# Kernel tuning notes

Hardware: AMD Instinct MI355X
Metric: run time of the kernel (lower is better)

## Reference

```python
import jax, jax.numpy as jnp
import numpy as np

KNOWN_POINTS = 8
TAU = 1.0


def setup_inputs() -> dict:
    key = jax.random.key(0)
    k1, k2, k3 = jax.random.split(key, 3)
    B, N, H = 8, 56564, 256
    return {
        "x": jax.random.normal(k1, (B, N), dtype=jnp.float32),
        "point_weight": jax.random.normal(k2, (1, N), dtype=jnp.float32),
        "weight": jax.random.normal(k3, (1, N, H), dtype=jnp.float32),
        "bias": jnp.zeros((1, H), dtype=jnp.float32),
    }


def _softmax_point_selection(point_weight, B, tau):
    """Iterative straight-through HardSoftmax top-k selection (stage=2).
    Returns a (B, N) {0,1}-valued mask (with straight-through softmax grads)."""
    N = point_weight.shape[1]
    weights = jnp.broadcast_to(point_weight, (B, N))  # repeat_interleave over batch
    minimum = jax.lax.stop_gradient(jnp.min(weights))
    total = jnp.zeros((B, N), dtype=weights.dtype)
    for _ in range(KNOWN_POINTS):
        soft = jax.nn.softmax(weights / tau, axis=1)
        hard = jax.nn.one_hot(jnp.argmax(weights, axis=1), N, dtype=weights.dtype)
        # straight-through: forward = hard, backward = softmax jacobian
        one_hot = hard - jax.lax.stop_gradient(soft) + soft
        total = total + one_hot
        # masked_fill at selected positions (no grad through filled entries)
        weights = jnp.where(hard > 0, minimum - 10000.0, weights)
    return total


def reference(x, point_weight, weight, bias):
    B = x.shape[0]
    mask = _softmax_point_selection(point_weight, B, TAU)  # (B, N)
    # out[b,h] = sum_n x[b,n] * mask[b,n] * W[n,h] + bias[h]
    # (equivalent to masking the (B,N,H) weight then matmul, without materializing it)
    out = jnp.einsum('bn,nh->bh', x * mask, weight[0]) + bias
    return out
```

## Files before the change

### kernel.cpp

```cpp
#include <hip/hip_runtime.h>

#define TPB 256
#define KSEL 8

__device__ __forceinline__ unsigned long long make_key(float v, unsigned int idx) {
    unsigned int u = __float_as_uint(v);
    unsigned int ord = (u & 0x80000000u) ? ~u : (u | 0x80000000u);
    return ((unsigned long long)ord << 32) | (unsigned long long)(~idx);
}

__device__ __forceinline__ unsigned long long kmax(unsigned long long a, unsigned long long b) {
    return a > b ? a : b;
}

__global__ __launch_bounds__(TPB) void topk_scan(const float* __restrict__ pw, int N,
                                                 unsigned long long* __restrict__ ws_keys) {
    __shared__ unsigned long long s_wave[TPB / 64];
    __shared__ unsigned long long s_win;
    __shared__ unsigned long long s_sel[KSEL];

    const int tid  = threadIdx.x;
    const int lane = tid & 63;
    const int wave = tid >> 6;
    const int N4   = N >> 2;
    const int gid  = blockIdx.x * TPB + tid;

    unsigned long long cand[5] = {0ull, 0ull, 0ull, 0ull, 0ull};
    if (gid < N4) {
        const float4 v = reinterpret_cast<const float4*>(pw)[gid];
        const unsigned int base = (unsigned int)gid * 4u;
        cand[0] = make_key(v.x, base + 0u);
        cand[1] = make_key(v.y, base + 1u);
        cand[2] = make_key(v.z, base + 2u);
        cand[3] = make_key(v.w, base + 3u);
    }
    if (blockIdx.x == 0) {
        int t = N4 * 4 + tid;
        if (t < N) cand[4] = make_key(pw[t], (unsigned int)t);
    }

    for (int p = 0; p < KSEL; ++p) {
        unsigned long long k = cand[0];
        #pragma unroll
        for (int c = 1; c < 5; ++c) k = kmax(k, cand[c]);
        #pragma unroll
        for (int o = 32; o > 0; o >>= 1) k = kmax(k, __shfl_down(k, o));
        if (lane == 0) s_wave[wave] = k;
        __syncthreads();
        if (tid == 0) {
            unsigned long long w = s_wave[0];
            #pragma unroll
            for (int i = 1; i < TPB / 64; ++i) w = kmax(w, s_wave[i]);
            s_win = w;
            s_sel[p] = w;
        }
        __syncthreads();
        const unsigned long long w = s_win;
        #pragma unroll
        for (int c = 0; c < 5; ++c) if (cand[c] == w) cand[c] = 0ull;
    }

    if (tid < KSEL) ws_keys[blockIdx.x * KSEL + tid] = s_sel[tid];
}

__global__ __launch_bounds__(TPB) void topk_merge_out(
        const unsigned long long* __restrict__ ws_keys, int nkeys,
        const float* __restrict__ x, const float* __restrict__ w,
        const float* __restrict__ bias, float* __restrict__ out,
        int N, int H, int B) {
    __shared__ unsigned long long s_wave[TPB / 64];
    __shared__ unsigned long long s_win;
    __shared__ int s_idx[KSEL];
    __shared__ float s_x[16][KSEL];

    const int tid  = threadIdx.x;
    const int lane = tid & 63;
    const int wave = tid >> 6;

    unsigned long long cand[2] = {0ull, 0ull};
    if (tid < nkeys)        cand[0] = ws_keys[tid];
    if (tid + TPB < nkeys)  cand[1] = ws_keys[tid + TPB];

    for (int p = 0; p < KSEL; ++p) {
        unsigned long long k = kmax(cand[0], cand[1]);
        #pragma unroll
        for (int o = 32; o > 0; o >>= 1) k = kmax(k, __shfl_down(k, o));
        if (lane == 0) s_wave[wave] = k;
        __syncthreads();
        if (tid == 0) {
            unsigned long long win = s_wave[0];
            #pragma unroll
            for (int i = 1; i < TPB / 64; ++i) win = kmax(win, s_wave[i]);
            s_win = win;
            s_idx[p] = (int)(~(unsigned int)(win & 0xffffffffull));
        }
        __syncthreads();
        const unsigned long long win = s_win;
        if (cand[0] == win) cand[0] = 0ull;
        if (cand[1] == win) cand[1] = 0ull;
    }

    __syncthreads();
    if (tid < B * KSEL) {
        const int b = tid / KSEL, k = tid % KSEL;
        s_x[b][k] = x[(long)b * N + s_idx[k]];
    }
    __syncthreads();

    for (int h = tid; h < H; h += TPB) {
        float wv[KSEL];
        #pragma unroll
        for (int k = 0; k < KSEL; ++k) wv[k] = w[(long)s_idx[k] * H + h];
        const float bv = bias[h];
        for (int b = 0; b < B; ++b) {
            float acc = bv;
            #pragma unroll
            for (int k = 0; k < KSEL; ++k) acc += s_x[b][k] * wv[k];
            out[(long)b * H + h] = acc;
        }
    }
}

extern "C" void kernel_launch(void* const* d_in, const int* in_sizes, int n_in,
                              void* d_out, int out_size, void* d_ws, size_t ws_size,
                              hipStream_t stream) {
    const float* x    = (const float*)d_in[0];
    const float* pw   = (const float*)d_in[1];
    const float* w    = (const float*)d_in[2];
    const float* bias = (const float*)d_in[3];
    float* out = (float*)d_out;

    const int N = in_sizes[1];
    const int H = in_sizes[3];
    const int B = in_sizes[0] / N;
    const int N4 = N >> 2;
    const int nblk = (N4 + TPB - 1) / TPB;

    unsigned long long* keys = (unsigned long long*)d_ws;

    topk_scan<<<nblk, TPB, 0, stream>>>(pw, N, keys);
    topk_merge_out<<<1, TPB, 0, stream>>>(keys, nblk * KSEL, x, w, bias, out, N, H, B);
}
```

Before: 16.90 us.

## Fuse top-k scan and output into single 1024-thread block kernel

Replaces the two-kernel scheme (many-block partial top-8 scan plus single-block merge) with one 1024-thread single-block kernel. Each thread keeps a running top-2 over its register-buffered slice, waves extract top-8 through xor shuffles and rescan only when a thread's two candidates are used up, and one wave merges the per-wave results. This removes a kernel launch and the workspace round trip. The cost is that a single CU must stream the whole 56K-element vector, and rare full rescans can make it slower.

```diff
diff --git a/kernel.cpp b/kernel.cpp
--- a/kernel.cpp
+++ b/kernel.cpp
@@ -1,122 +1,164 @@
 #include <hip/hip_runtime.h>
+#include <math.h>
 
-#define TPB 256
+#define TPB 1024
 #define KSEL 8
+#define MAXCHUNK 14
 
 __device__ __forceinline__ unsigned long long make_key(float v, unsigned int idx) {
     unsigned int u = __float_as_uint(v);
-    unsigned int ord = (u & 0x80000000u) ? ~u : (u | 0x80000000u);
+    unsigned int ord = u ^ ((unsigned int)((int)u >> 31) | 0x80000000u);
     return ((unsigned long long)ord << 32) | (unsigned long long)(~idx);
 }
 
-__device__ __forceinline__ unsigned long long kmax(unsigned long long a, unsigned long long b) {
-    return a > b ? a : b;
-}
-
-__global__ __launch_bounds__(TPB) void topk_scan(const float* __restrict__ pw, int N,
-                                                 unsigned long long* __restrict__ ws_keys) {
-    __shared__ unsigned long long s_wave[TPB / 64];
-    __shared__ unsigned long long s_win;
-    __shared__ unsigned long long s_sel[KSEL];
-
-    const int tid  = threadIdx.x;
-    const int lane = tid & 63;
-    const int wave = tid >> 6;
-    const int N4   = N >> 2;
-    const int gid  = blockIdx.x * TPB + tid;
-
-    unsigned long long cand[5] = {0ull, 0ull, 0ull, 0ull, 0ull};
-    if (gid < N4) {
-        const float4 v = reinterpret_cast<const float4*>(pw)[gid];
-        const unsigned int base = (unsigned int)gid * 4u;
-        cand[0] = make_key(v.x, base + 0u);
-        cand[1] = make_key(v.y, base + 1u);
-        cand[2] = make_key(v.z, base + 2u);
-        cand[3] = make_key(v.w, base + 3u);
-    }
-    if (blockIdx.x == 0) {
-        int t = N4 * 4 + tid;
-        if (t < N) cand[4] = make_key(pw[t], (unsigned int)t);
-    }
-
-    for (int p = 0; p < KSEL; ++p) {
-        unsigned long long k = cand[0];
-        #pragma unroll
-        for (int c = 1; c < 5; ++c) k = kmax(k, cand[c]);
-        #pragma unroll
-        for (int o = 32; o > 0; o >>= 1) k = kmax(k, __shfl_down(k, o));
-        if (lane == 0) s_wave[wave] = k;
-        __syncthreads();
-        if (tid == 0) {
-            unsigned long long w = s_wave[0];
-            #pragma unroll
-            for (int i = 1; i < TPB / 64; ++i) w = kmax(w, s_wave[i]);
-            s_win = w;
-            s_sel[p] = w;
-        }
-        __syncthreads();
-        const unsigned long long w = s_win;
-        #pragma unroll
-        for (int c = 0; c < 5; ++c) if (cand[c] == w) cand[c] = 0ull;
-    }
-
-    if (tid < KSEL) ws_keys[blockIdx.x * KSEL + tid] = s_sel[tid];
-}
-
-__global__ __launch_bounds__(TPB) void topk_merge_out(
-        const unsigned long long* __restrict__ ws_keys, int nkeys,
-        const float* __restrict__ x, const float* __restrict__ w,
-        const float* __restrict__ bias, float* __restrict__ out,
-        int N, int H, int B) {
-    __shared__ unsigned long long s_wave[TPB / 64];
-    __shared__ unsigned long long s_win;
+__global__ __launch_bounds__(TPB, 1) void fused_topk_linear(
+        const float* __restrict__ x, const float* __restrict__ pw,
+        const float* __restrict__ w, const float* __restrict__ bias,
+        float* __restrict__ out, int N, int H, int B) {
+    __shared__ unsigned long long s_wavekeys[(TPB / 64) * KSEL];
     __shared__ int s_idx[KSEL];
     __shared__ float s_x[16][KSEL];
 
     const int tid  = threadIdx.x;
     const int lane = tid & 63;
-    const int wave = tid >> 6;
+    const int wid  = tid >> 6;
+    const int N4   = N >> 2;
+    const int tail = N - (N4 << 2);
+    const float4* __restrict__ pw4 = reinterpret_cast<const float4*>(pw);
 
-    unsigned long long cand[2] = {0ull, 0ull};
-    if (tid < nkeys)        cand[0] = ws_keys[tid];
-    if (tid + TPB < nkeys)  cand[1] = ws_keys[tid + TPB];
-
-    for (int p = 0; p < KSEL; ++p) {
-        unsigned long long k = kmax(cand[0], cand[1]);
-        #pragma unroll
-        for (int o = 32; o > 0; o >>= 1) k = kmax(k, __shfl_down(k, o));
-        if (lane == 0) s_wave[wave] = k;
-        __syncthreads();
-        if (tid == 0) {
-            unsigned long long win = s_wave[0];
-            #pragma unroll
-            for (int i = 1; i < TPB / 64; ++i) win = kmax(win, s_wave[i]);
-            s_win = win;
-            s_idx[p] = (int)(~(unsigned int)(win & 0xffffffffull));
-        }
-        __syncthreads();
-        const unsigned long long win = s_win;
-        if (cand[0] == win) cand[0] = 0ull;
-        if (cand[1] == win) cand[1] = 0ull;
+    float4 buf[MAXCHUNK];
+    #pragma unroll
+    for (int j = 0; j < MAXCHUNK; ++j) {
+        int p = tid + j * TPB;
+        int pp = (p < N4) ? p : 0;
+        buf[j] = pw4[pp];
     }
 
-    __syncthreads();
-    if (tid < B * KSEL) {
-        const int b = tid / KSEL, k = tid % KSEL;
-        s_x[b][k] = x[(long)b * N + s_idx[k]];
+    float m1 = -INFINITY, m2 = -INFINITY;
+    unsigned int i1 = 0u, i2 = 0u;
+    #pragma unroll
+    for (int j = 0; j < MAXCHUNK; ++j) {
+        int p = tid + j * TPB;
+        bool valid = (p < N4);
+        float f[4] = {buf[j].x, buf[j].y, buf[j].z, buf[j].w};
+        unsigned int base = (unsigned int)p * 4u;
+        #pragma unroll
+        for (int c = 0; c < 4; ++c) {
+            float v = valid ? f[c] : -INFINITY;
+            unsigned int gi = base + (unsigned int)c;
+            bool gt = (v > m1);
+            float        lv = gt ? m1 : v;
+            unsigned int li = gt ? i1 : gi;
+            m1 = gt ? v  : m1;
+            i1 = gt ? gi : i1;
+            bool gt2 = (lv > m2);
+            m2 = gt2 ? lv : m2;
+            i2 = gt2 ? li : i2;
+        }
+    }
+    for (int p = tid + MAXCHUNK * TPB; p < N4; p += TPB) {
+        float4 v4 = pw4[p];
+        float f[4] = {v4.x, v4.y, v4.z, v4.w};
+        unsigned int base = (unsigned int)p * 4u;
+        #pragma unroll
+        for (int c = 0; c < 4; ++c) {
+            float v = f[c]; unsigned int gi = base + (unsigned int)c;
+            bool gt = (v > m1);
+            float lv = gt ? m1 : v; unsigned int li = gt ? i1 : gi;
+            m1 = gt ? v : m1; i1 = gt ? gi : i1;
+            bool gt2 = (lv > m2);
+            m2 = gt2 ? lv : m2; i2 = gt2 ? li : i2;
+        }
+    }
+    if (tid < tail) {
+        unsigned int gi = (unsigned int)(N4 * 4 + tid);
+        float v = pw[gi];
+        bool gt = (v > m1);
+        float lv = gt ? m1 : v; unsigned int li = gt ? i1 : gi;
+        m1 = gt ? v : m1; i1 = gt ? gi : i1;
+        bool gt2 = (lv > m2);
+        m2 = gt2 ? lv : m2; i2 = gt2 ? li : i2;
+    }
+
+    unsigned long long k1 = (m1 == -INFINITY) ? 0ull : make_key(m1, i1);
+    unsigned long long k2 = (m2 == -INFINITY) ? 0ull : make_key(m2, i2);
+
+    #pragma unroll 1
+    for (int p = 0; p < KSEL; ++p) {
+        unsigned long long wmax = k1;
+        #pragma unroll
+        for (int o = 32; o > 0; o >>= 1) {
+            unsigned long long other = __shfl_xor(wmax, o, 64);
+            if (other > wmax) wmax = other;
+        }
+        if (lane == 0) s_wavekeys[wid * KSEL + p] = wmax;
+        if (k1 == wmax && wmax != 0ull) {
+            unsigned long long nk = k2;
+            if (nk == 0ull) {
+                for (int q = tid; q < N4; q += TPB) {
+                    float4 v4 = pw4[q];
+                    float f[4] = {v4.x, v4.y, v4.z, v4.w};
+                    unsigned int base = (unsigned int)q * 4u;
+                    #pragma unroll
+                    for (int c = 0; c < 4; ++c) {
+                        unsigned long long k = make_key(f[c], base + (unsigned int)c);
+                        if (k < wmax && k > nk) nk = k;
+                    }
+                }
+                if (tid < tail) {
+                    unsigned int gi = (unsigned int)(N4 * 4 + tid);
+                    unsigned long long k = make_key(pw[gi], gi);
+                    if (k < wmax && k > nk) nk = k;
+                }
+            }
+            k1 = nk;
+            k2 = 0ull;
+        }
     }
     __syncthreads();
 
-    for (int h = tid; h < H; h += TPB) {
+    if (wid == 0) {
+        unsigned long long c0 = s_wavekeys[lane * 2];
+        unsigned long long c1 = s_wavekeys[lane * 2 + 1];
+        #pragma unroll 1
+        for (int p = 0; p < KSEL; ++p) {
+            unsigned long long m = (c0 > c1) ? c0 : c1;
+            #pragma unroll
+            for (int o = 32; o > 0; o >>= 1) {
+                unsigned long long other = __shfl_xor(m, o, 64);
+                if (other > m) m = other;
+            }
+            if (lane == 0) s_idx[p] = (int)(~(unsigned int)(m & 0xffffffffull));
+            if (c0 == m) c0 = 0ull;
+            if (c1 == m) c1 = 0ull;
+        }
+    }
+    __syncthreads();
+
+    if (tid < B * KSEL) {
+        int b = tid >> 3, k = tid & 7;
+        s_x[b][k] = x[(size_t)b * N + s_idx[k]];
+    }
+    __syncthreads();
+
+    int groups = TPB / H;
+    if (groups < 1) groups = 1;
+    int h = tid % H;
+    int g = tid / H;
+    if (g < groups && h < H) {
+        int bpg = (B + groups - 1) / groups;
         float wv[KSEL];
         #pragma unroll
-        for (int k = 0; k < KSEL; ++k) wv[k] = w[(long)s_idx[k] * H + h];
-        const float bv = bias[h];
-        for (int b = 0; b < B; ++b) {
-            float acc = bv;
-            #pragma unroll
-            for (int k = 0; k < KSEL; ++k) acc += s_x[b][k] * wv[k];
-            out[(long)b * H + h] = acc;
+        for (int k = 0; k < KSEL; ++k) wv[k] = w[(size_t)s_idx[k] * H + h];
+        float bv = bias[h];
+        for (int bb = 0; bb < bpg; ++bb) {
+            int b = g * bpg + bb;
+            if (b < B) {
+                float acc = bv;
+                #pragma unroll
+                for (int k = 0; k < KSEL; ++k) acc += s_x[b][k] * wv[k];
+                out[(size_t)b * H + h] = acc;
+            }
         }
     }
 }
@@ -133,11 +175,6 @@
     const int N = in_sizes[1];
     const int H = in_sizes[3];
     const int B = in_sizes[0] / N;
-    const int N4 = N >> 2;
-    const int nblk = (N4 + TPB - 1) / TPB;
 
-    unsigned long long* keys = (unsigned long long*)d_ws;
-
-    topk_scan<<<nblk, TPB, 0, stream>>>(pw, N, keys);
-    topk_merge_out<<<1, TPB, 0, stream>>>(keys, nblk * KSEL, x, w, bias, out, N, H, B);
+    fused_topk_linear<<<1, TPB, 0, stream>>>(x, pw, w, bias, out, N, H, B);
 }
```

Measured after the change: 20.59 us. 1.22x slower.

## Fuse top-k scan and merge into one kernel with last-block atomic

Applied to the files above, without the earlier changes.

Merges the two launches into a single kernel. The last block to finish, detected with an atomic counter and thread fences, performs the global merge and the small output GEMV. Per-block selection now uses a wave-local top-8 via xor shuffles followed by a single-wave merge, which removes the per-iteration block barriers. A memset is added to reset the counter each call, and correctness now depends on fence ordering.

```diff
diff --git a/kernel.cpp b/kernel.cpp
--- a/kernel.cpp
+++ b/kernel.cpp
@@ -1,4 +1,5 @@
 #include <hip/hip_runtime.h>
+#include <math.h>
 
 #define TPB 256
 #define KSEL 8
@@ -13,16 +14,32 @@
     return a > b ? a : b;
 }
 
-__global__ __launch_bounds__(TPB) void topk_scan(const float* __restrict__ pw, int N,
-                                                 unsigned long long* __restrict__ ws_keys) {
-    __shared__ unsigned long long s_wave[TPB / 64];
-    __shared__ unsigned long long s_win;
-    __shared__ unsigned long long s_sel[KSEL];
+__device__ __forceinline__ unsigned long long wave_kmax(unsigned long long k) {
+    #pragma unroll
+    for (int o = 32; o > 0; o >>= 1) {
+        unsigned long long other = __shfl_xor(k, o, 64);
+        k = kmax(k, other);
+    }
+    return k;
+}
+
+__global__ __launch_bounds__(TPB) void fused_topk_linear(
+        const float* __restrict__ x, const float* __restrict__ pw,
+        const float* __restrict__ w, const float* __restrict__ bias,
+        float* __restrict__ out,
+        unsigned long long* __restrict__ ws_keys,
+        unsigned int* __restrict__ counter,
+        int N, int H, int B, int nblk) {
+    __shared__ unsigned long long s_wk[(TPB / 64) * KSEL];
+    __shared__ int s_idx[KSEL];
+    __shared__ float s_x[16][KSEL];
+    __shared__ unsigned int s_rank;
 
     const int tid  = threadIdx.x;
     const int lane = tid & 63;
-    const int wave = tid >> 6;
+    const int wid  = tid >> 6;
     const int N4   = N >> 2;
+    const int tailN = N - (N4 << 2);
     const int gid  = blockIdx.x * TPB + tid;
 
     unsigned long long cand[5] = {0ull, 0ull, 0ull, 0ull, 0ull};
@@ -34,89 +51,76 @@
         cand[2] = make_key(v.z, base + 2u);
         cand[3] = make_key(v.w, base + 3u);
     }
-    if (blockIdx.x == 0) {
-        int t = N4 * 4 + tid;
-        if (t < N) cand[4] = make_key(pw[t], (unsigned int)t);
+    if (blockIdx.x == 0 && tid < tailN) {
+        const unsigned int gi = (unsigned int)(N4 * 4 + tid);
+        cand[4] = make_key(pw[gi], gi);
     }
 
+    #pragma unroll 1
     for (int p = 0; p < KSEL; ++p) {
-        unsigned long long k = cand[0];
+        unsigned long long k = kmax(kmax(kmax(cand[0], cand[1]), kmax(cand[2], cand[3])), cand[4]);
+        k = wave_kmax(k);
+        if (lane == 0) s_wk[wid * KSEL + p] = k;
         #pragma unroll
-        for (int c = 1; c < 5; ++c) k = kmax(k, cand[c]);
-        #pragma unroll
-        for (int o = 32; o > 0; o >>= 1) k = kmax(k, __shfl_down(k, o));
-        if (lane == 0) s_wave[wave] = k;
-        __syncthreads();
-        if (tid == 0) {
-            unsigned long long w = s_wave[0];
-            #pragma unroll
-            for (int i = 1; i < TPB / 64; ++i) w = kmax(w, s_wave[i]);
-            s_win = w;
-            s_sel[p] = w;
+        for (int c = 0; c < 5; ++c) if (cand[c] == k) cand[c] = 0ull;
+    }
+    __syncthreads();
+
+    if (wid == 0) {
+        unsigned long long c0 = (lane < (TPB / 64) * KSEL) ? s_wk[lane] : 0ull;
+        #pragma unroll 1
+        for (int p = 0; p < KSEL; ++p) {
+            unsigned long long m = wave_kmax(c0);
+            if (lane == 0) ws_keys[blockIdx.x * KSEL + p] = m;
+            if (c0 == m) c0 = 0ull;
         }
-        __syncthreads();
-        const unsigned long long w = s_win;
-        #pragma unroll
-        for (int c = 0; c < 5; ++c) if (cand[c] == w) cand[c] = 0ull;
     }
 
-    if (tid < KSEL) ws_keys[blockIdx.x * KSEL + tid] = s_sel[tid];
-}
+    __threadfence();
+    if (tid == 0) s_rank = atomicAdd(counter, 1u);
+    __syncthreads();
+    if (s_rank != (unsigned int)(nblk - 1)) return;
+    __threadfence();
 
-__global__ __launch_bounds__(TPB) void topk_merge_out(
-        const unsigned long long* __restrict__ ws_keys, int nkeys,
-        const float* __restrict__ x, const float* __restrict__ w,
-        const float* __restrict__ bias, float* __restrict__ out,
-        int N, int H, int B) {
-    __shared__ unsigned long long s_wave[TPB / 64];
-    __shared__ unsigned long long s_win;
-    __shared__ int s_idx[KSEL];
-    __shared__ float s_x[16][KSEL];
+    const int nk = nblk * KSEL;
+    const int k0i = wid * 128 + lane * 2;
+    unsigned long long c0 = (k0i < nk)     ? ws_keys[k0i]     : 0ull;
+    unsigned long long c1 = (k0i + 1 < nk) ? ws_keys[k0i + 1] : 0ull;
+    #pragma unroll 1
+    for (int p = 0; p < KSEL; ++p) {
+        unsigned long long m = wave_kmax(kmax(c0, c1));
+        if (lane == 0) s_wk[wid * KSEL + p] = m;
+        if (c0 == m) c0 = 0ull;
+        if (c1 == m) c1 = 0ull;
+    }
+    __syncthreads();
+    if (wid == 0) {
+        unsigned long long c = (lane < (TPB / 64) * KSEL) ? s_wk[lane] : 0ull;
+        #pragma unroll 1
+        for (int p = 0; p < KSEL; ++p) {
+            unsigned long long m = wave_kmax(c);
+            if (lane == 0) s_idx[p] = (int)(~(unsigned int)(m & 0xffffffffull));
+            if (c == m) c = 0ull;
+        }
+    }
+    __syncthreads();
 
-    const int tid  = threadIdx.x;
-    const int lane = tid & 63;
-    const int wave = tid >> 6;
-
-    unsigned long long cand[2] = {0ull, 0ull};
-    if (tid < nkeys)        cand[0] = ws_keys[tid];
-    if (tid + TPB < nkeys)  cand[1] = ws_keys[tid + TPB];
-
-    for (int p = 0; p < KSEL; ++p) {
-        unsigned long long k = kmax(cand[0], cand[1]);
-        #pragma unroll
-        for (int o = 32; o > 0; o >>= 1) k = kmax(k, __shfl_down(k, o));
-        if (lane == 0) s_wave[wave] = k;
-        __syncthreads();
-        if (tid == 0) {
-            unsigned long long win = s_wave[0];
-            #pragma unroll
-            for (int i = 1; i < TPB / 64; ++i) win = kmax(win, s_wave[i]);
-            s_win = win;
-            s_idx[p] = (int)(~(unsigned int)(win & 0xffffffffull));
-        }
-        __syncthreads();
-        const unsigned long long win = s_win;
-        if (cand[0] == win) cand[0] = 0ull;
-        if (cand[1] == win) cand[1] = 0ull;
-    }
-
-    __syncthreads();
     if (tid < B * KSEL) {
-        const int b = tid / KSEL, k = tid % KSEL;
-        s_x[b][k] = x[(long)b * N + s_idx[k]];
+        const int b = tid >> 3, k = tid & 7;
+        s_x[b][k] = x[(size_t)b * N + s_idx[k]];
     }
     __syncthreads();
 
     for (int h = tid; h < H; h += TPB) {
         float wv[KSEL];
         #pragma unroll
-        for (int k = 0; k < KSEL; ++k) wv[k] = w[(long)s_idx[k] * H + h];
+        for (int k = 0; k < KSEL; ++k) wv[k] = w[(size_t)s_idx[k] * H + h];
         const float bv = bias[h];
         for (int b = 0; b < B; ++b) {
             float acc = bv;
             #pragma unroll
             for (int k = 0; k < KSEL; ++k) acc += s_x[b][k] * wv[k];
-            out[(long)b * H + h] = acc;
+            out[(size_t)b * H + h] = acc;
         }
     }
 }
@@ -136,8 +140,10 @@
     const int N4 = N >> 2;
     const int nblk = (N4 + TPB - 1) / TPB;
 
-    unsigned long long* keys = (unsigned long long*)d_ws;
+    unsigned int* counter = (unsigned int*)d_ws;
+    unsigned long long* keys = (unsigned long long*)((char*)d_ws + 256);
 
-    topk_scan<<<nblk, TPB, 0, stream>>>(pw, N, keys);
-    topk_merge_out<<<1, TPB, 0, stream>>>(keys, nblk * KSEL, x, w, bias, out, N, H, B);
+    hipMemsetAsync(counter, 0, sizeof(unsigned int), stream);
+    fused_topk_linear<<<nblk, TPB, 0, stream>>>(x, pw, w, bias, out,
+                                                keys, counter, N, H, B, nblk);
 }
```

New measurement: 26.06 us. 54.2% more time.
